# Kernel tuning notes

Hardware: AMD Instinct MI355X
Metric: run time of the kernel (lower is better)

## Reference

```python
import jax, jax.numpy as jnp
import numpy as np

M = 16384            # total tokens in batch (s)
MAX_RANK = 64        # K, max LoRA rank
NUM_SLICES = 2       # fused output slices (<=3 per kernel static_assert)
OUTPUT_DIM = 4096    # N
NUM_LORA = 8         # number of adapters
NUM_SEGMENTS = 8     # contiguous logical segments, one adapter each


def setup_inputs() -> dict:
    key = jax.random.key(0)
    k1, k2, k3, k4, k5 = jax.random.split(key, 5)
    x = jax.random.normal(k1, (M, NUM_SLICES * MAX_RANK), dtype=jnp.float32)
    weights = jax.random.normal(k2, (NUM_LORA, OUTPUT_DIM, MAX_RANK), dtype=jnp.float32) * 0.02
    # equal-length segments covering all M tokens
    seg_indptr = jnp.arange(NUM_SEGMENTS + 1, dtype=jnp.int32) * (M // NUM_SEGMENTS)
    weight_indices = jax.random.randint(k3, (NUM_SEGMENTS,), 0, NUM_LORA, dtype=jnp.int32)
    # variable per-adapter ranks, including a rank-0 (no-op) adapter
    lora_ranks = jnp.array([64, 32, 16, 0, 64, 48, 64, 32], dtype=jnp.int32)
    scalings = jax.random.uniform(k4, (NUM_LORA,), dtype=jnp.float32, minval=0.25, maxval=2.0)
    permutation = jax.random.permutation(k5, M).astype(jnp.int32)
    slice_offsets = jnp.array([0, OUTPUT_DIM // 2, OUTPUT_DIM], dtype=jnp.int32)
    return dict(x=x, weights=weights, seg_indptr=seg_indptr,
                weight_indices=weight_indices, lora_ranks=lora_ranks,
                scalings=scalings, permutation=permutation,
                slice_offsets=slice_offsets, num_segments=NUM_SEGMENTS)


def reference(x, weights, seg_indptr, weight_indices, lora_ranks, scalings,
              permutation, slice_offsets, num_segments):
    M_, D = x.shape
    num_lora, out_dim, max_rank = weights.shape
    num_slices = slice_offsets.shape[0] - 1
    xp = x[permutation]                     # rows in logical (segment) order: (M, D)
    logical = jnp.arange(M_)
    kk = jnp.arange(max_rank)
    nn = jnp.arange(out_dim)
    acc = jnp.zeros((M_, out_dim), dtype=x.dtype)   # accumulated in logical order
    for s in range(num_segments):
        w = weight_indices[s]
        r = lora_ranks[w]                   # actual rank of this segment's adapter
        scal = scalings[w].astype(x.dtype)
        in_seg = (logical >= seg_indptr[s]) & (logical < seg_indptr[s + 1]) & (r > 0)
        W = weights[w]                      # (OUTPUT_DIM, MAX_RANK)
        seg_acc = jnp.zeros((M_, out_dim), dtype=x.dtype)
        for j in range(num_slices):
            kmask = kk < r                  # only first r of MAX_RANK columns are live
            cols = jnp.where(kmask, j * r + kk, 0)   # x packed at slice_id * cur_rank
            xsub = xp[:, cols] * kmask.astype(x.dtype)        # (M, MAX_RANK)
            nmask = ((nn >= slice_offsets[j]) & (nn < slice_offsets[j + 1])).astype(x.dtype)
            seg_acc = seg_acc + (xsub @ W.T) * (scal * nmask)  # (M, OUTPUT_DIM)
        acc = acc + jnp.where(in_seg[:, None], seg_acc, 0.0)
    # scatter back from logical order to physical row positions
    out = jnp.zeros((M_, out_dim), dtype=x.dtype).at[permutation].add(acc)
    return out
```

## Files before the change

kernel.cpp:

```cpp
#include <hip/hip_runtime.h>

typedef float  f32x2v __attribute__((ext_vector_type(2)));
typedef float  f32x16 __attribute__((ext_vector_type(16)));
typedef __bf16 bf16x8 __attribute__((ext_vector_type(8)));

constexpr int D_IN   = 128;
constexpr int KMAX   = 64;
constexpr int N_OUT  = 4096;
constexpr int NSLICE = 2;

constexpr int BM = 128;
constexpr int BN = 128;
constexpr int THREADS = 256;

constexpr size_t WBF_OFF = 0;
constexpr size_t XBF_OFF = 8u << 20;

__device__ __forceinline__ unsigned short f2bf(float f) {
    unsigned u = __builtin_bit_cast(unsigned, f);
    u += 0x7fffu + ((u >> 16) & 1u);
    return (unsigned short)(u >> 16);
}
__device__ __forceinline__ unsigned pk2(float a, float b) {
    return (unsigned)f2bf(a) | ((unsigned)f2bf(b) << 16);
}

__global__ __launch_bounds__(256)
void conv_w(const float* __restrict__ w, unsigned* __restrict__ wbf, int npairs) {
    int i = blockIdx.x * 256 + threadIdx.x;
    if (i >= npairs) return;
    f32x2v v = *(const f32x2v*)&w[(size_t)i * 2];
    wbf[i] = pk2(v.x, v.y);
}

__global__ __launch_bounds__(256)
void conv_x(const float* __restrict__ x,
            const int*   __restrict__ seg_indptr,
            const int*   __restrict__ weight_indices,
            const int*   __restrict__ lora_ranks,
            const float* __restrict__ scalings,
            const int*   __restrict__ permutation,
            unsigned* __restrict__ xbf,
            int num_segments, int m_tok)
{
    const int idx = blockIdx.x * 256 + threadIdx.x;
    const int l   = idx >> 6;
    if (l >= m_tok) return;
    const int c   = (idx & 63) * 2;
    const int j   = c >> 6;
    const int k   = c & 63;

    int s = 0;
    for (int i = 0; i < num_segments; ++i)
        if (l >= seg_indptr[i] && l < seg_indptr[i + 1]) s = i;
    const int   w    = weight_indices[s];
    const int   r    = lora_ranks[w];
    const float scal = scalings[w];

    const int p = permutation[l];
    float v0 = 0.f, v1 = 0.f;
    if (k < r)     v0 = scal * x[(size_t)p * D_IN + j * r + k];
    if (k + 1 < r) v1 = scal * x[(size_t)p * D_IN + j * r + k + 1];
    xbf[idx] = pk2(v0, v1);
}

__global__ __launch_bounds__(THREADS, 4)
void lora_mfma(const __bf16* __restrict__ xbf,
               const __bf16* __restrict__ wbf,
               const int*    __restrict__ seg_indptr,
               const int*    __restrict__ weight_indices,
               const int*    __restrict__ permutation,
               const int*    __restrict__ slice_offsets,
               float* __restrict__ out,
               int num_segments, int n_slices)
{
    __shared__ int Ps[BM];

    const int t    = threadIdx.x;
    const int row0 = blockIdx.y * BM;
    const int col0 = blockIdx.x * BN;

    if (t < BM) Ps[t] = permutation[row0 + t];
    __syncthreads();

    int s = 0;
    for (int i = 0; i < num_segments; ++i)
        if (row0 >= seg_indptr[i] && row0 < seg_indptr[i + 1]) s = i;
    const int w = weight_indices[s];

    int j = 0;
    for (int i = 1; i < n_slices; ++i) j += (col0 >= slice_offsets[i]);

    const int lane = t & 63;
    const int wv   = t >> 6;
    const int wm   = wv & 1;
    const int wn   = wv >> 1;
    const int half = lane >> 5;
    const int l32  = lane & 31;

    const __bf16* __restrict__ Xb =
        xbf + ((size_t)(row0 + wm * 64 + l32) * NSLICE + j) * KMAX + half * 8;
    const __bf16* __restrict__ Wb =
        wbf + ((size_t)w * N_OUT + col0 + wn * 64 + l32) * KMAX + half * 8;

    f32x16 acc[2][2] = {};

    #pragma unroll
    for (int ks = 0; ks < 4; ++ks) {
        const int kof = ks * 16;
        bf16x8 a0 = *(const bf16x8*)&Xb[kof];
        bf16x8 a1 = *(const bf16x8*)&Xb[(size_t)32 * NSLICE * KMAX + kof];
        bf16x8 b0 = *(const bf16x8*)&Wb[kof];
        bf16x8 b1 = *(const bf16x8*)&Wb[(size_t)32 * KMAX + kof];
        acc[0][0] = __builtin_amdgcn_mfma_f32_32x32x16_bf16(a0, b0, acc[0][0], 0, 0, 0);
        acc[0][1] = __builtin_amdgcn_mfma_f32_32x32x16_bf16(a0, b1, acc[0][1], 0, 0, 0);
        acc[1][0] = __builtin_amdgcn_mfma_f32_32x32x16_bf16(a1, b0, acc[1][0], 0, 0, 0);
        acc[1][1] = __builtin_amdgcn_mfma_f32_32x32x16_bf16(a1, b1, acc[1][1], 0, 0, 0);
    }

    #pragma unroll
    for (int mt = 0; mt < 2; ++mt) {
        #pragma unroll
        for (int reg = 0; reg < 16; ++reg) {
            const int m = wm * 64 + mt * 32 + (reg & 3) + 8 * (reg >> 2) + 4 * half;
            float* op = &out[(size_t)Ps[m] * N_OUT + col0 + wn * 64 + l32];
            op[0]  = acc[mt][0][reg];
            op[32] = acc[mt][1][reg];
        }
    }
}

extern "C" void kernel_launch(void* const* d_in, const int* in_sizes, int n_in,
                              void* d_out, int out_size, void* d_ws, size_t ws_size,
                              hipStream_t stream) {
    (void)n_in; (void)out_size; (void)ws_size;
    const float* x              = (const float*)d_in[0];
    const float* weights        = (const float*)d_in[1];
    const int*   seg_indptr     = (const int*)d_in[2];
    const int*   weight_indices = (const int*)d_in[3];
    const int*   lora_ranks     = (const int*)d_in[4];
    const float* scalings       = (const float*)d_in[5];
    const int*   permutation    = (const int*)d_in[6];
    const int*   slice_offsets  = (const int*)d_in[7];
    float*       out            = (float*)d_out;

    const int num_segments = in_sizes[2] - 1;
    const int n_slices     = in_sizes[7] - 1;
    const int m_tok        = in_sizes[6];
    const int w_elems      = in_sizes[1];

    unsigned* wbf = (unsigned*)((char*)d_ws + WBF_OFF);
    unsigned* xbf = (unsigned*)((char*)d_ws + XBF_OFF);

    const int wpairs = w_elems / 2;
    conv_w<<<(wpairs + 255) / 256, 256, 0, stream>>>(weights, wbf, wpairs);

    const int xthreads = m_tok * (NSLICE * KMAX / 2);
    conv_x<<<(xthreads + 255) / 256, 256, 0, stream>>>(
        x, seg_indptr, weight_indices, lora_ranks, scalings, permutation,
        xbf, num_segments, m_tok);

    dim3 grid(N_OUT / BN, m_tok / BM);
    lora_mfma<<<grid, THREADS, 0, stream>>>(
        (const __bf16*)xbf, (const __bf16*)wbf, seg_indptr, weight_indices,
        permutation, slice_offsets, out, num_segments, n_slices);
}
```

Before: 305.4 us.

## Fuse bf16 conversion kernels into the LoRA MFMA kernel

Drops the separate weight and activation conversion kernels and their workspace buffers. The MFMA kernel now gathers permuted fp32 rows of x and fp32 weights directly, converts them to bf16 in registers, and applies the adapter scaling in the epilogue. It also skips the MFMA loop entirely for rank-0 adapters and masks K chunks beyond the adapter rank. The cost is reading fp32 data, twice the bytes, with uncoalesced gathered rows of x inside the main kernel, plus lowering the occupancy hint from 4 to 3.

```diff
diff --git a/kernel.cpp b/kernel.cpp
--- a/kernel.cpp
+++ b/kernel.cpp
@@ -1,78 +1,36 @@
 #include <hip/hip_runtime.h>
 
-typedef float  f32x2v __attribute__((ext_vector_type(2)));
+typedef float  f32x4  __attribute__((ext_vector_type(4)));
 typedef float  f32x16 __attribute__((ext_vector_type(16)));
 typedef __bf16 bf16x8 __attribute__((ext_vector_type(8)));
 
 constexpr int D_IN   = 128;
 constexpr int KMAX   = 64;
 constexpr int N_OUT  = 4096;
-constexpr int NSLICE = 2;
 
 constexpr int BM = 128;
 constexpr int BN = 128;
 constexpr int THREADS = 256;
 
-constexpr size_t WBF_OFF = 0;
-constexpr size_t XBF_OFF = 8u << 20;
 
-__device__ __forceinline__ unsigned short f2bf(float f) {
-    unsigned u = __builtin_bit_cast(unsigned, f);
-    u += 0x7fffu + ((u >> 16) & 1u);
-    return (unsigned short)(u >> 16);
-}
-__device__ __forceinline__ unsigned pk2(float a, float b) {
-    return (unsigned)f2bf(a) | ((unsigned)f2bf(b) << 16);
+__device__ __forceinline__ bf16x8 cvt8(f32x4 a, f32x4 b) {
+    bf16x8 r;
+    r[0] = (__bf16)a.x; r[1] = (__bf16)a.y; r[2] = (__bf16)a.z; r[3] = (__bf16)a.w;
+    r[4] = (__bf16)b.x; r[5] = (__bf16)b.y; r[6] = (__bf16)b.z; r[7] = (__bf16)b.w;
+    return r;
 }
 
-__global__ __launch_bounds__(256)
-void conv_w(const float* __restrict__ w, unsigned* __restrict__ wbf, int npairs) {
-    int i = blockIdx.x * 256 + threadIdx.x;
-    if (i >= npairs) return;
-    f32x2v v = *(const f32x2v*)&w[(size_t)i * 2];
-    wbf[i] = pk2(v.x, v.y);
-}
-
-__global__ __launch_bounds__(256)
-void conv_x(const float* __restrict__ x,
-            const int*   __restrict__ seg_indptr,
-            const int*   __restrict__ weight_indices,
-            const int*   __restrict__ lora_ranks,
-            const float* __restrict__ scalings,
-            const int*   __restrict__ permutation,
-            unsigned* __restrict__ xbf,
-            int num_segments, int m_tok)
-{
-    const int idx = blockIdx.x * 256 + threadIdx.x;
-    const int l   = idx >> 6;
-    if (l >= m_tok) return;
-    const int c   = (idx & 63) * 2;
-    const int j   = c >> 6;
-    const int k   = c & 63;
-
-    int s = 0;
-    for (int i = 0; i < num_segments; ++i)
-        if (l >= seg_indptr[i] && l < seg_indptr[i + 1]) s = i;
-    const int   w    = weight_indices[s];
-    const int   r    = lora_ranks[w];
-    const float scal = scalings[w];
-
-    const int p = permutation[l];
-    float v0 = 0.f, v1 = 0.f;
-    if (k < r)     v0 = scal * x[(size_t)p * D_IN + j * r + k];
-    if (k + 1 < r) v1 = scal * x[(size_t)p * D_IN + j * r + k + 1];
-    xbf[idx] = pk2(v0, v1);
-}
-
-__global__ __launch_bounds__(THREADS, 4)
-void lora_mfma(const __bf16* __restrict__ xbf,
-               const __bf16* __restrict__ wbf,
-               const int*    __restrict__ seg_indptr,
-               const int*    __restrict__ weight_indices,
-               const int*    __restrict__ permutation,
-               const int*    __restrict__ slice_offsets,
-               float* __restrict__ out,
-               int num_segments, int n_slices)
+__global__ __launch_bounds__(THREADS, 3)
+void lora_fused(const float* __restrict__ x,
+                const float* __restrict__ wgt,
+                const int*   __restrict__ seg_indptr,
+                const int*   __restrict__ weight_indices,
+                const int*   __restrict__ lora_ranks,
+                const float* __restrict__ scalings,
+                const int*   __restrict__ permutation,
+                const int*   __restrict__ slice_offsets,
+                float* __restrict__ out,
+                int num_segments, int n_slices)
 {
     __shared__ int Ps[BM];
 
@@ -86,7 +44,9 @@
     int s = 0;
     for (int i = 0; i < num_segments; ++i)
         if (row0 >= seg_indptr[i] && row0 < seg_indptr[i + 1]) s = i;
-    const int w = weight_indices[s];
+    const int   wa   = weight_indices[s];
+    const int   r    = lora_ranks[wa];
+    const float scal = scalings[wa];
 
     int j = 0;
     for (int i = 1; i < n_slices; ++i) j += (col0 >= slice_offsets[i]);
@@ -98,24 +58,41 @@
     const int half = lane >> 5;
     const int l32  = lane & 31;
 
-    const __bf16* __restrict__ Xb =
-        xbf + ((size_t)(row0 + wm * 64 + l32) * NSLICE + j) * KMAX + half * 8;
-    const __bf16* __restrict__ Wb =
-        wbf + ((size_t)w * N_OUT + col0 + wn * 64 + l32) * KMAX + half * 8;
-
     f32x16 acc[2][2] = {};
 
-    #pragma unroll
-    for (int ks = 0; ks < 4; ++ks) {
-        const int kof = ks * 16;
-        bf16x8 a0 = *(const bf16x8*)&Xb[kof];
-        bf16x8 a1 = *(const bf16x8*)&Xb[(size_t)32 * NSLICE * KMAX + kof];
-        bf16x8 b0 = *(const bf16x8*)&Wb[kof];
-        bf16x8 b1 = *(const bf16x8*)&Wb[(size_t)32 * KMAX + kof];
-        acc[0][0] = __builtin_amdgcn_mfma_f32_32x32x16_bf16(a0, b0, acc[0][0], 0, 0, 0);
-        acc[0][1] = __builtin_amdgcn_mfma_f32_32x32x16_bf16(a0, b1, acc[0][1], 0, 0, 0);
-        acc[1][0] = __builtin_amdgcn_mfma_f32_32x32x16_bf16(a1, b0, acc[1][0], 0, 0, 0);
-        acc[1][1] = __builtin_amdgcn_mfma_f32_32x32x16_bf16(a1, b1, acc[1][1], 0, 0, 0);
+    if (r > 0) {
+        const float* __restrict__ xb0 =
+            x + (size_t)Ps[wm * 64 + l32]      * D_IN + j * r + half * 8;
+        const float* __restrict__ xb1 =
+            x + (size_t)Ps[wm * 64 + 32 + l32] * D_IN + j * r + half * 8;
+        const float* __restrict__ wb =
+            wgt + ((size_t)wa * N_OUT + col0 + wn * 64 + l32) * KMAX + half * 8;
+
+        #pragma unroll
+        for (int ks = 0; ks < 4; ++ks) {
+            const int  kof = ks * 16;
+            const bool pv  = (half * 8 + kof + 8) <= r;
+            const f32x4 z  = {0.f, 0.f, 0.f, 0.f};
+
+            f32x4 a0lo = pv ? *(const f32x4*)(xb0 + kof)     : z;
+            f32x4 a0hi = pv ? *(const f32x4*)(xb0 + kof + 4) : z;
+            f32x4 a1lo = pv ? *(const f32x4*)(xb1 + kof)     : z;
+            f32x4 a1hi = pv ? *(const f32x4*)(xb1 + kof + 4) : z;
+            f32x4 b0lo = *(const f32x4*)(wb + kof);
+            f32x4 b0hi = *(const f32x4*)(wb + kof + 4);
+            f32x4 b1lo = *(const f32x4*)(wb + (size_t)32 * KMAX + kof);
+            f32x4 b1hi = *(const f32x4*)(wb + (size_t)32 * KMAX + kof + 4);
+
+            bf16x8 A0 = cvt8(a0lo, a0hi);
+            bf16x8 A1 = cvt8(a1lo, a1hi);
+            bf16x8 B0 = cvt8(b0lo, b0hi);
+            bf16x8 B1 = cvt8(b1lo, b1hi);
+
+            acc[0][0] = __builtin_amdgcn_mfma_f32_32x32x16_bf16(A0, B0, acc[0][0], 0, 0, 0);
+            acc[0][1] = __builtin_amdgcn_mfma_f32_32x32x16_bf16(A0, B1, acc[0][1], 0, 0, 0);
+            acc[1][0] = __builtin_amdgcn_mfma_f32_32x32x16_bf16(A1, B0, acc[1][0], 0, 0, 0);
+            acc[1][1] = __builtin_amdgcn_mfma_f32_32x32x16_bf16(A1, B1, acc[1][1], 0, 0, 0);
+        }
     }
 
     #pragma unroll
@@ -124,8 +101,8 @@
         for (int reg = 0; reg < 16; ++reg) {
             const int m = wm * 64 + mt * 32 + (reg & 3) + 8 * (reg >> 2) + 4 * half;
             float* op = &out[(size_t)Ps[m] * N_OUT + col0 + wn * 64 + l32];
-            op[0]  = acc[mt][0][reg];
-            op[32] = acc[mt][1][reg];
+            op[0]  = scal * acc[mt][0][reg];
+            op[32] = scal * acc[mt][1][reg];
         }
     }
 }
@@ -133,7 +110,7 @@
 extern "C" void kernel_launch(void* const* d_in, const int* in_sizes, int n_in,
                               void* d_out, int out_size, void* d_ws, size_t ws_size,
                               hipStream_t stream) {
-    (void)n_in; (void)out_size; (void)ws_size;
+    (void)n_in; (void)out_size; (void)d_ws; (void)ws_size;
     const float* x              = (const float*)d_in[0];
     const float* weights        = (const float*)d_in[1];
     const int*   seg_indptr     = (const int*)d_in[2];
@@ -147,21 +124,9 @@
     const int num_segments = in_sizes[2] - 1;
     const int n_slices     = in_sizes[7] - 1;
     const int m_tok        = in_sizes[6];
-    const int w_elems      = in_sizes[1];
-
-    unsigned* wbf = (unsigned*)((char*)d_ws + WBF_OFF);
-    unsigned* xbf = (unsigned*)((char*)d_ws + XBF_OFF);
-
-    const int wpairs = w_elems / 2;
-    conv_w<<<(wpairs + 255) / 256, 256, 0, stream>>>(weights, wbf, wpairs);
-
-    const int xthreads = m_tok * (NSLICE * KMAX / 2);
-    conv_x<<<(xthreads + 255) / 256, 256, 0, stream>>>(
-        x, seg_indptr, weight_indices, lora_ranks, scalings, permutation,
-        xbf, num_segments, m_tok);
 
     dim3 grid(N_OUT / BN, m_tok / BM);
-    lora_mfma<<<grid, THREADS, 0, stream>>>(
-        (const __bf16*)xbf, (const __bf16*)wbf, seg_indptr, weight_indices,
+    lora_fused<<<grid, THREADS, 0, stream>>>(
+        x, weights, seg_indptr, weight_indices, lora_ranks, scalings,
         permutation, slice_offsets, out, num_segments, n_slices);
 }
```

Measured after the change: 314.5 us. 1.03x slower.
